# Performance work log

Measured on AMD Instinct MI355X. Metric: run time of the kernel, lower is better.

## Reference

```python
import jax, jax.numpy as jnp
import numpy as np

B, S, D = 8, 2048, 512

def setup_inputs() -> dict:
    key = jax.random.key(0)
    ks = jax.random.split(key, 9)
    scale = 1.0 / np.sqrt(D)
    q = jax.random.normal(ks[0], (B, S, D), dtype=jnp.float32)
    k = jax.random.normal(ks[1], (B, S, D), dtype=jnp.float32)
    v = jax.random.normal(ks[2], (B, S, D), dtype=jnp.float32)
    # causal mask, broadcast over batch: True = attend
    mask = jnp.tril(jnp.ones((S, S), dtype=bool))[None, :, :]
    Wq = jax.random.normal(ks[3], (D, D), dtype=jnp.float32) * scale
    bq = jax.random.normal(ks[4], (D,), dtype=jnp.float32) * scale
    Wk = jax.random.normal(ks[5], (D, D), dtype=jnp.float32) * scale
    bk = jax.random.normal(ks[6], (D,), dtype=jnp.float32) * scale
    Wv = jax.random.normal(ks[7], (D, D), dtype=jnp.float32) * scale
    bv = jax.random.normal(ks[8], (D,), dtype=jnp.float32) * scale
    return {"q": q, "k": k, "v": v, "mask": mask,
            "Wq": Wq, "bq": bq, "Wk": Wk, "bk": bk, "Wv": Wv, "bv": bv}

def reference(q, k, v, mask, Wq, bq, Wk, bk, Wv, bv):
    # torch nn.Linear: x @ W^T + b
    Q = jnp.einsum('bsd,ed->bse', q, Wq) + bq
    K = jnp.einsum('bsd,ed->bse', k, Wk) + bk
    V = jnp.einsum('bsd,ed->bse', v, Wv) + bv
    scores = jnp.einsum('bqd,bkd->bqk', Q, K) / jnp.sqrt(jnp.float32(D))
    scores = jnp.where(mask, scores, jnp.float32(-1e9))
    prob = jax.nn.softmax(scores, axis=-1)
    out = jnp.einsum('bqk,bkd->bqd', prob, V)
    return out
```

## Files before the change

kernel.cpp:

```cpp
#include <hip/hip_runtime.h>
#include <stdint.h>
#include <stddef.h>
#include <math.h>

typedef _Float16 half8 __attribute__((ext_vector_type(8)));
typedef float f32x4 __attribute__((ext_vector_type(4)));

#define SCALE_QK 0.04419417382415922f

__device__ __forceinline__ void gload16(const void* g, void* lds) {
  __builtin_amdgcn_global_load_lds(
      (const __attribute__((address_space(1))) void*)g,
      (__attribute__((address_space(3))) void*)lds,
      16, 0, 0);
}

template<bool A_F32>
__device__ __forceinline__ void run_kloop(const void* Arow0, const _Float16* Brow0,
                                          int lda, int ldb, int kIters,
                                          _Float16* As, _Float16 (*Bs)[128*64],
                                          f32x4 (&acc)[4][4])
{
  const int tid  = threadIdx.x;
  const int lane = tid & 63;
  const int w    = tid >> 6;
  const int wm   = w >> 1, wn = w & 1;
  const int srow = tid >> 3;
  const int sg   = tid & 7;
  const int swz  = sg ^ (srow & 7);
  const int fr   = lane & 15;
  const int fq   = lane >> 4;
  const int fx   = lane & 7;

  f32x4 preF[8];
  half8 preH[4];

  auto loadA = [&](int it) {
    const int k0 = it * 64;
    if constexpr (A_F32) {
      const float* A = (const float*)Arow0;
      #pragma unroll
      for (int i = 0; i < 4; ++i) {
        const float* src = A + (size_t)(i*32 + srow) * lda + (k0 + sg*8);
        preF[2*i]   = *(const f32x4*)src;
        preF[2*i+1] = *(const f32x4*)(src + 4);
      }
    } else {
      const _Float16* A = (const _Float16*)Arow0;
      #pragma unroll
      for (int i = 0; i < 4; ++i)
        preH[i] = *(const half8*)(A + (size_t)(i*32 + srow) * lda + (k0 + sg*8));
    }
  };
  auto writeA = [&]() {
    #pragma unroll
    for (int i = 0; i < 4; ++i) {
      half8 h;
      if constexpr (A_F32) {
        f32x4 x = preF[2*i], y = preF[2*i+1];
        h[0]=(_Float16)x[0]; h[1]=(_Float16)x[1]; h[2]=(_Float16)x[2]; h[3]=(_Float16)x[3];
        h[4]=(_Float16)y[0]; h[5]=(_Float16)y[1]; h[6]=(_Float16)y[2]; h[7]=(_Float16)y[3];
      } else {
        h = preH[i];
      }
      *(half8*)(As + (i*32 + srow)*64 + swz*8) = h;
    }
  };
  auto gloadB = [&](int it, _Float16* dstBs) {
    const int k0 = it * 64;
    #pragma unroll
    for (int i = 0; i < 4; ++i)
      gload16(Brow0 + (size_t)(i*32 + srow) * ldb + (k0 + swz*8), dstBs + i*2048 + w*512);
  };
  auto compute = [&](const _Float16* cBs) {
    #pragma unroll
    for (int ks = 0; ks < 2; ++ks) {
      half8 av[4], bv[4];
      const int slot = (ks*4 + fq) ^ fx;
      #pragma unroll
      for (int i = 0; i < 4; ++i) {
        av[i] = *(const half8*)(As + (wm*64 + i*16 + fr)*64 + slot*8);
        bv[i] = *(const half8*)(cBs + (wn*64 + i*16 + fr)*64 + slot*8);
      }
      #pragma unroll
      for (int i = 0; i < 4; ++i) {
        #pragma unroll
        for (int j = 0; j < 4; ++j)
          acc[i][j] = __builtin_amdgcn_mfma_f32_16x16x32_f16(av[i], bv[j], acc[i][j], 0, 0, 0);
      }
    }
  };

  loadA(0);
  gloadB(0, Bs[0]);
  writeA();
  __syncthreads();

  for (int it = 0; it < kIters; ++it) {
    const int cur = it & 1;
    const bool more = (it + 1) < kIters;
    if (more) {
      gloadB(it + 1, Bs[cur ^ 1]);
      loadA(it + 1);
    }
    compute(Bs[cur]);
    __syncthreads();
    if (more) writeA();
    __syncthreads();
  }
}

__global__ __launch_bounds__(256) void k_cvtw(const float* __restrict__ Wq,
                                              const float* __restrict__ Wk,
                                              const float* __restrict__ Wv,
                                              _Float16* __restrict__ Wb)
{
  const int t = blockIdx.x * 256 + threadIdx.x;
  const int base = t * 8;
  const int z = base >> 18;
  const int off = base & 262143;
  const float* src = (z == 0) ? Wq : ((z == 1) ? Wk : Wv);
  f32x4 a = *(const f32x4*)(src + off);
  f32x4 b = *(const f32x4*)(src + off + 4);
  half8 h;
  h[0]=(_Float16)a[0]; h[1]=(_Float16)a[1]; h[2]=(_Float16)a[2]; h[3]=(_Float16)a[3];
  h[4]=(_Float16)b[0]; h[5]=(_Float16)b[1]; h[6]=(_Float16)b[2]; h[7]=(_Float16)b[3];
  *(half8*)(Wb + base) = h;
}

__global__ __launch_bounds__(256) void k_proj(const float* __restrict__ q,
                                              const float* __restrict__ k,
                                              const float* __restrict__ v,
                                              const _Float16* __restrict__ Wb,
                                              const float* __restrict__ bq,
                                              const float* __restrict__ bk,
                                              const float* __restrict__ bv,
                                              _Float16* __restrict__ Qb,
                                              _Float16* __restrict__ Kb,
                                              _Float16* __restrict__ Vb)
{
  __shared__ __align__(16) _Float16 As[128*64];
  __shared__ __align__(16) _Float16 Bs[2][128*64];
  const int bid = blockIdx.x;
  const int xcd = bid & 7, i = bid >> 3;
  const int p = xcd * 48 + (i >> 2);
  const int nt = i & 3;
  const int z = p >> 7, mt = p & 127;

  const float* A     = (z == 0) ? q  : (z == 1) ? k  : v;
  const float* bia   = (z == 0) ? bq : (z == 1) ? bk : bv;
  const _Float16* B  = Wb + (size_t)z * 512 * 512;
  _Float16* C        = (z == 0) ? Qb : (z == 1) ? Kb : Vb;

  f32x4 acc[4][4] = {};
  run_kloop<true>(A + (size_t)mt*128*512, B + (size_t)nt*128*512, 512, 512, 8, As, Bs, acc);

  const int lane = threadIdx.x & 63, w = threadIdx.x >> 6;
  const int wm = w >> 1, wn = w & 1;
  const int fr = lane & 15, fq = lane >> 4;
  #pragma unroll
  for (int j = 0; j < 4; ++j) {
    const int col = nt*128 + wn*64 + j*16 + fr;
    const float bval = bia[col];
    #pragma unroll
    for (int i2 = 0; i2 < 4; ++i2) {
      const int row = mt*128 + wm*64 + i2*16 + fq*4;
      #pragma unroll
      for (int r = 0; r < 4; ++r)
        C[(size_t)(row + r) * 512 + col] = (_Float16)(acc[i2][j][r] + bval);
    }
  }
}

__global__ __launch_bounds__(256) void k_trans(const _Float16* __restrict__ Vb,
                                               _Float16* __restrict__ Vt)
{
  __shared__ __align__(16) _Float16 t[64][72];
  const int st = blockIdx.x, dt = blockIdx.y, b = blockIdx.z;
  const int r = threadIdx.x >> 2, g = threadIdx.x & 3;
  const _Float16* src = Vb + ((size_t)b*2048 + st*64 + r)*512 + dt*64 + g*16;
  half8 v0 = *(const half8*)src;
  half8 v1 = *(const half8*)(src + 8);
  *(half8*)&t[r][g*16]     = v0;
  *(half8*)&t[r][g*16 + 8] = v1;
  __syncthreads();
  half8 o0, o1;
  #pragma unroll
  for (int i2 = 0; i2 < 8; ++i2) o0[i2] = t[g*16 + i2][r];
  #pragma unroll
  for (int i2 = 0; i2 < 8; ++i2) o1[i2] = t[g*16 + 8 + i2][r];
  _Float16* dst = Vt + ((size_t)b*512 + dt*64 + r)*2048 + st*64 + g*16;
  *(half8*)dst       = o0;
  *(half8*)(dst + 8) = o1;
}

__global__ __launch_bounds__(256) void k_scores(const _Float16* __restrict__ Qb,
                                                const _Float16* __restrict__ Kb,
                                                _Float16* __restrict__ P)
{
  const int bid = blockIdx.x;
  const int b = bid & 7;
  const int t = bid >> 3;
  int qt = (int)((sqrtf(8.0f * (float)t + 1.0f) - 1.0f) * 0.5f);
  int base = (qt * (qt + 1)) >> 1;
  if (t < base)                { --qt; base = (qt * (qt + 1)) >> 1; }
  else if (t >= base + qt + 1) { ++qt; base = (qt * (qt + 1)) >> 1; }
  const int kt = t - base;

  __shared__ __align__(16) _Float16 As[128*64];
  __shared__ __align__(16) _Float16 Bs[2][128*64];
  f32x4 acc[4][4] = {};
  run_kloop<false>(Qb + ((size_t)b*2048 + qt*128)*512,
                   Kb + ((size_t)b*2048 + kt*128)*512,
                   512, 512, 8, As, Bs, acc);
  const int lane = threadIdx.x & 63, w = threadIdx.x >> 6;
  const int wm = w >> 1, wn = w & 1;
  const int fr = lane & 15, fq = lane >> 4;
  #pragma unroll
  for (int i = 0; i < 4; ++i) {
    const int row = qt*128 + wm*64 + i*16 + fq*4;
    #pragma unroll
    for (int j = 0; j < 4; ++j) {
      const int col = kt*128 + wn*64 + j*16 + fr;
      #pragma unroll
      for (int r = 0; r < 4; ++r)
        P[((size_t)b*2048 + row + r) * 2048 + col] = (_Float16)(acc[i][j][r] * SCALE_QK);
    }
  }
}

__global__ __launch_bounds__(256) void k_softmax(_Float16* __restrict__ P)
{
  const int lane = threadIdx.x & 63;
  const int row  = blockIdx.x * 4 + (threadIdx.x >> 6);
  const int qIdx = row & 2047;
  _Float16* p = P + (size_t)row * 2048;
  const int L    = qIdx + 1;
  const int Lpad = ((qIdx >> 7) + 1) * 128;

  float m = -1e30f, s = 0.f;
  for (int i0 = lane * 8; i0 < L; i0 += 512) {
    float xv[8];
    if (i0 + 8 <= L) {
      half8 x = *(const half8*)(p + i0);
      #pragma unroll
      for (int j = 0; j < 8; ++j) xv[j] = (float)x[j];
    } else {
      #pragma unroll
      for (int j = 0; j < 8; ++j) xv[j] = (i0 + j < L) ? (float)p[i0 + j] : -1e30f;
    }
    float cm = xv[0];
    #pragma unroll
    for (int j = 1; j < 8; ++j) cm = fmaxf(cm, xv[j]);
    const float mn = fmaxf(m, cm);
    float cs = 0.f;
    #pragma unroll
    for (int j = 0; j < 8; ++j) cs += __expf(xv[j] - mn);
    s = s * __expf(m - mn) + cs;
    m = mn;
  }
  #pragma unroll
  for (int d = 1; d < 64; d <<= 1) {
    const float mo = __shfl_xor(m, d, 64);
    const float so = __shfl_xor(s, d, 64);
    const float mn = fmaxf(m, mo);
    s = s * __expf(m - mn) + so * __expf(mo - mn);
    m = mn;
  }
  const float inv = 1.0f / s;

  for (int i0 = lane * 8; i0 < Lpad; i0 += 512) {
    half8 o;
    if (i0 + 8 <= L) {
      half8 x = *(const half8*)(p + i0);
      #pragma unroll
      for (int j = 0; j < 8; ++j) o[j] = (_Float16)(__expf((float)x[j] - m) * inv);
    } else {
      #pragma unroll
      for (int j = 0; j < 8; ++j) {
        const int idx = i0 + j;
        o[j] = (idx < L) ? (_Float16)(__expf((float)p[idx] - m) * inv) : (_Float16)0.f;
      }
    }
    *(half8*)(p + i0) = o;
  }
}

__global__ __launch_bounds__(256) void k_pv(const _Float16* __restrict__ P,
                                            const _Float16* __restrict__ Vt,
                                            float* __restrict__ Out)
{
  const int bid = blockIdx.x;
  const int b = bid & 7;
  const int r0 = bid >> 3;
  const int qi = r0 >> 2, dt = r0 & 3;
  const int qt = (qi & 1) ? (15 - (qi >> 1)) : (qi >> 1);

  __shared__ __align__(16) _Float16 As[128*64];
  __shared__ __align__(16) _Float16 Bs[2][128*64];
  f32x4 acc[4][4] = {};
  run_kloop<false>(P  + ((size_t)b*2048 + qt*128)*2048,
                   Vt + ((size_t)b*512  + dt*128)*2048,
                   2048, 2048, (qt + 1) * 2, As, Bs, acc);
  const int lane = threadIdx.x & 63, w = threadIdx.x >> 6;
  const int wm = w >> 1, wn = w & 1;
  const int fr = lane & 15, fq = lane >> 4;
  #pragma unroll
  for (int i = 0; i < 4; ++i) {
    const int row = qt*128 + wm*64 + i*16 + fq*4;
    #pragma unroll
    for (int j = 0; j < 4; ++j) {
      const int col = dt*128 + wn*64 + j*16 + fr;
      #pragma unroll
      for (int r = 0; r < 4; ++r)
        Out[((size_t)b*2048 + row + r) * 512 + col] = acc[i][j][r];
    }
  }
}

extern "C" void kernel_launch(void* const* d_in, const int* in_sizes, int n_in,
                              void* d_out, int out_size, void* d_ws, size_t ws_size,
                              hipStream_t stream) {
  (void)in_sizes; (void)n_in; (void)out_size;
  const float* q  = (const float*)d_in[0];
  const float* k  = (const float*)d_in[1];
  const float* v  = (const float*)d_in[2];
  const float* Wq = (const float*)d_in[4];
  const float* bq = (const float*)d_in[5];
  const float* Wk = (const float*)d_in[6];
  const float* bk = (const float*)d_in[7];
  const float* Wv = (const float*)d_in[8];
  const float* bv = (const float*)d_in[9];

  const size_t OFF_P  = 0;
  const size_t OFF_Q  = (size_t)64 << 20;
  const size_t OFF_K  = (size_t)80 << 20;
  const size_t OFF_V  = (size_t)96 << 20;
  const size_t OFF_VT = (size_t)112 << 20;
  const size_t OFF_W  = (size_t)128 << 20;
  const size_t NEEDED = OFF_W + (size_t)3 * 512 * 512 * sizeof(_Float16);
  if (ws_size < NEEDED) return;

  char* ws = (char*)d_ws;
  _Float16* P  = (_Float16*)(ws + OFF_P);
  _Float16* Qb = (_Float16*)(ws + OFF_Q);
  _Float16* Kb = (_Float16*)(ws + OFF_K);
  _Float16* Vb = (_Float16*)(ws + OFF_V);
  _Float16* Vt = (_Float16*)(ws + OFF_VT);
  _Float16* Wb = (_Float16*)(ws + OFF_W);
  float* Out = (float*)d_out;

  k_cvtw   <<<dim3(384),      dim3(256), 0, stream>>>(Wq, Wk, Wv, Wb);
  k_proj   <<<dim3(1536),     dim3(256), 0, stream>>>(q, k, v, Wb, bq, bk, bv, Qb, Kb, Vb);
  k_trans  <<<dim3(32, 8, 8), dim3(256), 0, stream>>>(Vb, Vt);
  k_scores <<<dim3(1088),     dim3(256), 0, stream>>>(Qb, Kb, P);
  k_softmax<<<dim3(4096),     dim3(256), 0, stream>>>(P);
  k_pv     <<<dim3(512),      dim3(256), 0, stream>>>(P, Vt, Out);
}
```

Before: 283.0 us.

## Double-buffer A tiles with direct-to-LDS loads and cache softmax row in registers

The GEMM k-loop now double-buffers both A and B tiles in LDS. For fp16 A operands it uses global_load_lds directly instead of staging through registers, and the loop is unrolled by two so each barrier is followed by a prefetch into the other buffer. This removes the register round-trip and the extra barrier-separated writeA for the scores and PV kernels, at the cost of doubling LDS for A, which may reduce occupancy. The softmax kernel also keeps the row chunks in registers between the max/sum pass and the normalize pass, avoiding a second global read. The unroll-by-two assumes kIters is even, which holds here.

```diff
diff --git a/kernel.cpp b/kernel.cpp
--- a/kernel.cpp
+++ b/kernel.cpp
@@ -18,7 +18,8 @@
 template<bool A_F32>
 __device__ __forceinline__ void run_kloop(const void* Arow0, const _Float16* Brow0,
                                           int lda, int ldb, int kIters,
-                                          _Float16* As, _Float16 (*Bs)[128*64],
+                                          _Float16* As0, _Float16* As1,
+                                          _Float16* Bs0, _Float16* Bs1,
                                           f32x4 (&acc)[4][4])
 {
   const int tid  = threadIdx.x;
@@ -33,53 +34,53 @@
   const int fx   = lane & 7;
 
   f32x4 preF[8];
-  half8 preH[4];
-
-  auto loadA = [&](int it) {
+
+  auto loadAreg = [&](int it) {
+    const float* A = (const float*)Arow0;
     const int k0 = it * 64;
-    if constexpr (A_F32) {
-      const float* A = (const float*)Arow0;
-      #pragma unroll
-      for (int i = 0; i < 4; ++i) {
-        const float* src = A + (size_t)(i*32 + srow) * lda + (k0 + sg*8);
-        preF[2*i]   = *(const f32x4*)src;
-        preF[2*i+1] = *(const f32x4*)(src + 4);
-      }
-    } else {
-      const _Float16* A = (const _Float16*)Arow0;
-      #pragma unroll
-      for (int i = 0; i < 4; ++i)
-        preH[i] = *(const half8*)(A + (size_t)(i*32 + srow) * lda + (k0 + sg*8));
-    }
-  };
-  auto writeA = [&]() {
     #pragma unroll
     for (int i = 0; i < 4; ++i) {
+      const float* src = A + (size_t)(i*32 + srow) * lda + (k0 + sg*8);
+      preF[2*i]   = *(const f32x4*)src;
+      preF[2*i+1] = *(const f32x4*)(src + 4);
+    }
+  };
+  auto writeA = [&](_Float16* dst) {
+    #pragma unroll
+    for (int i = 0; i < 4; ++i) {
+      f32x4 x = preF[2*i], y = preF[2*i+1];
       half8 h;
-      if constexpr (A_F32) {
-        f32x4 x = preF[2*i], y = preF[2*i+1];
-        h[0]=(_Float16)x[0]; h[1]=(_Float16)x[1]; h[2]=(_Float16)x[2]; h[3]=(_Float16)x[3];
-        h[4]=(_Float16)y[0]; h[5]=(_Float16)y[1]; h[6]=(_Float16)y[2]; h[7]=(_Float16)y[3];
-      } else {
-        h = preH[i];
-      }
-      *(half8*)(As + (i*32 + srow)*64 + swz*8) = h;
-    }
-  };
-  auto gloadB = [&](int it, _Float16* dstBs) {
+      h[0]=(_Float16)x[0]; h[1]=(_Float16)x[1]; h[2]=(_Float16)x[2]; h[3]=(_Float16)x[3];
+      h[4]=(_Float16)y[0]; h[5]=(_Float16)y[1]; h[6]=(_Float16)y[2]; h[7]=(_Float16)y[3];
+      *(half8*)(dst + (i*32 + srow)*64 + swz*8) = h;
+    }
+  };
+  auto gloadA = [&](int it, _Float16* dst) {
+    const _Float16* A = (const _Float16*)Arow0;
     const int k0 = it * 64;
     #pragma unroll
     for (int i = 0; i < 4; ++i)
-      gload16(Brow0 + (size_t)(i*32 + srow) * ldb + (k0 + swz*8), dstBs + i*2048 + w*512);
-  };
-  auto compute = [&](const _Float16* cBs) {
+      gload16(A + (size_t)(i*32 + srow) * lda + (k0 + swz*8), dst + i*2048 + w*512);
+  };
+  auto gloadB = [&](int it, _Float16* dst) {
+    const int k0 = it * 64;
+    #pragma unroll
+    for (int i = 0; i < 4; ++i)
+      gload16(Brow0 + (size_t)(i*32 + srow) * ldb + (k0 + swz*8), dst + i*2048 + w*512);
+  };
+  auto stage = [&](int it, _Float16* dA, _Float16* dB) {
+    if constexpr (A_F32) loadAreg(it);
+    else                 gloadA(it, dA);
+    gloadB(it, dB);
+  };
+  auto compute = [&](const _Float16* cAs, const _Float16* cBs) {
     #pragma unroll
     for (int ks = 0; ks < 2; ++ks) {
       half8 av[4], bv[4];
       const int slot = (ks*4 + fq) ^ fx;
       #pragma unroll
       for (int i = 0; i < 4; ++i) {
-        av[i] = *(const half8*)(As + (wm*64 + i*16 + fr)*64 + slot*8);
+        av[i] = *(const half8*)(cAs + (wm*64 + i*16 + fr)*64 + slot*8);
         bv[i] = *(const half8*)(cBs + (wn*64 + i*16 + fr)*64 + slot*8);
       }
       #pragma unroll
@@ -91,21 +92,19 @@
     }
   };
 
-  loadA(0);
-  gloadB(0, Bs[0]);
-  writeA();
+  stage(0, As0, Bs0);
+  if constexpr (A_F32) writeA(As0);
   __syncthreads();
 
-  for (int it = 0; it < kIters; ++it) {
-    const int cur = it & 1;
-    const bool more = (it + 1) < kIters;
-    if (more) {
-      gloadB(it + 1, Bs[cur ^ 1]);
-      loadA(it + 1);
-    }
-    compute(Bs[cur]);
+  for (int it = 0; it < kIters; it += 2) {
+    stage(it + 1, As1, Bs1);
+    compute(As0, Bs0);
+    if constexpr (A_F32) writeA(As1);
     __syncthreads();
-    if (more) writeA();
+    const bool more = (it + 2) < kIters;
+    if (more) stage(it + 2, As0, Bs0);
+    compute(As1, Bs1);
+    if constexpr (A_F32) { if (more) writeA(As0); }
     __syncthreads();
   }
 }
@@ -139,8 +138,8 @@
                                               _Float16* __restrict__ Kb,
                                               _Float16* __restrict__ Vb)
 {
-  __shared__ __align__(16) _Float16 As[128*64];
-  __shared__ __align__(16) _Float16 Bs[2][128*64];
+  __shared__ __align__(16) _Float16 As0[128*64], As1[128*64];
+  __shared__ __align__(16) _Float16 Bs0[128*64], Bs1[128*64];
   const int bid = blockIdx.x;
   const int xcd = bid & 7, i = bid >> 3;
   const int p = xcd * 48 + (i >> 2);
@@ -153,7 +152,8 @@
   _Float16* C        = (z == 0) ? Qb : (z == 1) ? Kb : Vb;
 
   f32x4 acc[4][4] = {};
-  run_kloop<true>(A + (size_t)mt*128*512, B + (size_t)nt*128*512, 512, 512, 8, As, Bs, acc);
+  run_kloop<true>(A + (size_t)mt*128*512, B + (size_t)nt*128*512, 512, 512, 8,
+                  As0, As1, Bs0, Bs1, acc);
 
   const int lane = threadIdx.x & 63, w = threadIdx.x >> 6;
   const int wm = w >> 1, wn = w & 1;
@@ -207,12 +207,12 @@
   else if (t >= base + qt + 1) { ++qt; base = (qt * (qt + 1)) >> 1; }
   const int kt = t - base;
 
-  __shared__ __align__(16) _Float16 As[128*64];
-  __shared__ __align__(16) _Float16 Bs[2][128*64];
+  __shared__ __align__(16) _Float16 As0[128*64], As1[128*64];
+  __shared__ __align__(16) _Float16 Bs0[128*64], Bs1[128*64];
   f32x4 acc[4][4] = {};
   run_kloop<false>(Qb + ((size_t)b*2048 + qt*128)*512,
                    Kb + ((size_t)b*2048 + kt*128)*512,
-                   512, 512, 8, As, Bs, acc);
+                   512, 512, 8, As0, As1, Bs0, Bs1, acc);
   const int lane = threadIdx.x & 63, w = threadIdx.x >> 6;
   const int wm = w >> 1, wn = w & 1;
   const int fr = lane & 15, fq = lane >> 4;
@@ -238,26 +238,27 @@
   const int L    = qIdx + 1;
   const int Lpad = ((qIdx >> 7) + 1) * 128;
 
+  half8 xb[4];
   float m = -1e30f, s = 0.f;
-  for (int i0 = lane * 8; i0 < L; i0 += 512) {
-    float xv[8];
-    if (i0 + 8 <= L) {
+  #pragma unroll
+  for (int c = 0; c < 4; ++c) {
+    const int i0 = lane * 8 + c * 512;
+    if (i0 < Lpad) {
       half8 x = *(const half8*)(p + i0);
-      #pragma unroll
-      for (int j = 0; j < 8; ++j) xv[j] = (float)x[j];
-    } else {
-      #pragma unroll
-      for (int j = 0; j < 8; ++j) xv[j] = (i0 + j < L) ? (float)p[i0 + j] : -1e30f;
-    }
-    float cm = xv[0];
-    #pragma unroll
-    for (int j = 1; j < 8; ++j) cm = fmaxf(cm, xv[j]);
-    const float mn = fmaxf(m, cm);
-    float cs = 0.f;
-    #pragma unroll
-    for (int j = 0; j < 8; ++j) cs += __expf(xv[j] - mn);
-    s = s * __expf(m - mn) + cs;
-    m = mn;
+      xb[c] = x;
+      float xv[8];
+      #pragma unroll
+      for (int j = 0; j < 8; ++j) xv[j] = (i0 + j < L) ? (float)x[j] : -1e30f;
+      float cm = xv[0];
+      #pragma unroll
+      for (int j = 1; j < 8; ++j) cm = fmaxf(cm, xv[j]);
+      const float mn = fmaxf(m, cm);
+      float cs = 0.f;
+      #pragma unroll
+      for (int j = 0; j < 8; ++j) cs += __expf(xv[j] - mn);
+      s = s * __expf(m - mn) + cs;
+      m = mn;
+    }
   }
   #pragma unroll
   for (int d = 1; d < 64; d <<= 1) {
@@ -269,20 +270,17 @@
   }
   const float inv = 1.0f / s;
 
-  for (int i0 = lane * 8; i0 < Lpad; i0 += 512) {
-    half8 o;
-    if (i0 + 8 <= L) {
-      half8 x = *(const half8*)(p + i0);
-      #pragma unroll
-      for (int j = 0; j < 8; ++j) o[j] = (_Float16)(__expf((float)x[j] - m) * inv);
-    } else {
-      #pragma unroll
-      for (int j = 0; j < 8; ++j) {
-        const int idx = i0 + j;
-        o[j] = (idx < L) ? (_Float16)(__expf((float)p[idx] - m) * inv) : (_Float16)0.f;
-      }
-    }
-    *(half8*)(p + i0) = o;
+  #pragma unroll
+  for (int c = 0; c < 4; ++c) {
+    const int i0 = lane * 8 + c * 512;
+    if (i0 < Lpad) {
+      half8 x = xb[c];
+      half8 o;
+      #pragma unroll
+      for (int j = 0; j < 8; ++j)
+        o[j] = (i0 + j < L) ? (_Float16)(__expf((float)x[j] - m) * inv) : (_Float16)0.f;
+      *(half8*)(p + i0) = o;
+    }
   }
 }
 
@@ -296,12 +294,12 @@
   const int qi = r0 >> 2, dt = r0 & 3;
   const int qt = (qi & 1) ? (15 - (qi >> 1)) : (qi >> 1);
 
-  __shared__ __align__(16) _Float16 As[128*64];
-  __shared__ __align__(16) _Float16 Bs[2][128*64];
+  __shared__ __align__(16) _Float16 As0[128*64], As1[128*64];
+  __shared__ __align__(16) _Float16 Bs0[128*64], Bs1[128*64];
   f32x4 acc[4][4] = {};
   run_kloop<false>(P  + ((size_t)b*2048 + qt*128)*2048,
                    Vt + ((size_t)b*512  + dt*128)*2048,
-                   2048, 2048, (qt + 1) * 2, As, Bs, acc);
+                   2048, 2048, (qt + 1) * 2, As0, As1, Bs0, Bs1, acc);
   const int lane = threadIdx.x & 63, w = threadIdx.x >> 6;
   const int wm = w >> 1, wn = w & 1;
   const int fr = lane & 15, fq = lane >> 4;
```

New measurement: 272.5 us. -3.7%, faster.
